# Performance work log

Measured on AMD Instinct MI355X. Metric: run time of the kernel, lower is better.

The kernel has to match this reference:

```python
import jax, jax.numpy as jnp
import numpy as np


def bilinear_align_corners(p, H, W):
    # p: [B, C, h, w] -> [B, C, H, W], matches F.interpolate(mode='bilinear', align_corners=True)
    b, c, h, w = p.shape
    ys = jnp.linspace(0.0, h - 1.0, H)
    xs = jnp.linspace(0.0, w - 1.0, W)
    y0 = jnp.floor(ys).astype(jnp.int32)
    x0 = jnp.floor(xs).astype(jnp.int32)
    y1 = jnp.minimum(y0 + 1, h - 1)
    x1 = jnp.minimum(x0 + 1, w - 1)
    wy = (ys - y0.astype(p.dtype))[:, None]          # [H,1]
    wx = (xs - x0.astype(p.dtype))                   # [W]
    rows = p[:, :, y0, :] * (1 - wy) + p[:, :, y1, :] * wy   # [B,C,H,w]
    out = rows[:, :, :, x0] * (1 - wx) + rows[:, :, :, x1] * wx  # [B,C,H,W]
    return out


def conv1x1(x, W, b):
    return jnp.einsum('bchw,oc->bohw', x, W) + b[None, :, None, None]


def scan_axis(feat, A_bar, B_bar, axis):
    # selective recurrence h_i = A_i * stop_grad(h_{i-1}) + B_i * x_i along `axis`
    f = jnp.moveaxis(feat, axis, 0)
    A = jnp.moveaxis(A_bar, axis, 0)
    B = jnp.moveaxis(B_bar, axis, 0)

    def step(prev, inp):
        a_i, b_i, x_i = inp
        h = a_i * jax.lax.stop_gradient(prev) + b_i * x_i
        return h, h

    _, hs = jax.lax.scan(step, jnp.zeros_like(f[0]), (A, B, f))
    return jnp.moveaxis(hs, 0, axis)


def setup_inputs() -> dict:
    key = jax.random.key(0)
    ks = jax.random.split(key, 12)
    Bsz, Cin, H, W = 4, 64, 256, 256
    hid = 128
    s_in = 1.0 / np.sqrt(Cin)
    s_hid = 1.0 / np.sqrt(hid)
    return {
        'x': jax.random.normal(ks[0], (Bsz, Cin, H, W), jnp.float32),
        'prior': jax.random.normal(ks[1], (Bsz, 1, 64, 64), jnp.float32),
        'W_in': jax.random.uniform(ks[2], (hid, Cin), jnp.float32, -s_in, s_in),
        'b_in': jax.random.uniform(ks[3], (hid,), jnp.float32, -s_in, s_in),
        'W_out': jax.random.uniform(ks[4], (Cin, hid), jnp.float32, -s_hid, s_hid),
        'b_out': jax.random.uniform(ks[5], (Cin,), jnp.float32, -s_hid, s_hid),
        'W_delta': jax.random.uniform(ks[6], (hid, hid), jnp.float32, -s_hid, s_hid),
        'b_delta': jax.random.uniform(ks[7], (hid,), jnp.float32, -s_hid, s_hid),
        'W_B': jax.random.uniform(ks[8], (hid, hid), jnp.float32, -s_hid, s_hid),
        'b_B': jax.random.uniform(ks[9], (hid,), jnp.float32, -s_hid, s_hid),
        'A_param': jax.random.normal(ks[10], (hid,), jnp.float32),
        'lambda_delta': jnp.float32(0.1),
        'alpha': jnp.float32(0.1),
        'gamma': jnp.float32(0.1),
    }


def reference(x, prior, W_in, b_in, W_out, b_out, W_delta, b_delta, W_B, b_B,
              A_param, lambda_delta, alpha, gamma):
    Bsz, C, H, W = x.shape
    prior_up = jnp.clip(bilinear_align_corners(prior, H, W), -1.0, 1.0)
    x_proj = conv1x1(x, W_in, b_in)
    delta = jax.nn.softplus(conv1x1(x_proj, W_delta, b_delta) + lambda_delta * prior_up)
    B_k = conv1x1(x_proj, W_B, b_B) * (1.0 + alpha * prior_up)
    A = -jnp.exp(A_param)[None, :, None, None]
    A_bar = jnp.exp(delta * A)
    B_bar = delta * B_k
    # dim=0 in torch code scans along W (axis 3); dim=1 scans along H (axis 2)
    scanned = scan_axis(x_proj, A_bar, B_bar, 3) + scan_axis(x_proj, A_bar, B_bar, 2)
    out = conv1x1(scanned, W_out, b_out)
    return (x + gamma * out, prior_up)
```

## Files before the change

### kernel.cpp

```cpp
#include <hip/hip_runtime.h>
#include <hip/hip_bf16.h>

#define OUT1 16777216
#define BIG  33554432

typedef _Float16 half8 __attribute__((ext_vector_type(8)));
typedef float    floatx4 __attribute__((ext_vector_type(4)));

struct __align__(8) h4s { _Float16 x, y, z, w; };
struct __align__(16) au16 { h4s a, u; };

__global__ __launch_bounds__(256) void k_prior(const float* __restrict__ prior, float* __restrict__ pu){
    int i = blockIdx.x*256 + threadIdx.x;
    int b = i >> 16;
    int rem = i & 65535;
    int yy = rem >> 8, xx = rem & 255;
    const float scale = 63.0f/255.0f;
    float sy = yy*scale, sx = xx*scale;
    int y0 = min((int)floorf(sy), 63), x0 = min((int)floorf(sx), 63);
    int y1 = min(y0+1, 63), x1 = min(x0+1, 63);
    float wy = sy - (float)y0, wx = sx - (float)x0;
    const float* pb = prior + (b<<12);
    float v00 = pb[(y0<<6)+x0], v01 = pb[(y0<<6)+x1];
    float v10 = pb[(y1<<6)+x0], v11 = pb[(y1<<6)+x1];
    float r0 = v00*(1.f-wy) + v10*wy;
    float r1 = v01*(1.f-wy) + v11*wy;
    float v  = r0*(1.f-wx) + r1*wx;
    pu[i] = fminf(fmaxf(v, -1.f), 1.f);
}

__global__ __launch_bounds__(256) void k_comb(const float* __restrict__ W_in, const float* __restrict__ b_in,
        const float* __restrict__ W_delta, const float* __restrict__ b_delta,
        const float* __restrict__ W_B, const float* __restrict__ b_B,
        const float* __restrict__ A_param, const float* __restrict__ W_out,
        _Float16* __restrict__ Wch, float* __restrict__ bcv, float* __restrict__ negA,
        _Float16* __restrict__ Wof, float* __restrict__ bct){
    int i = blockIdx.x*256 + threadIdx.x;
    if (i < 24576){
        int r = i >> 6, c = i & 63;
        float v;
        if (r < 128) v = W_in[i];
        else if (r < 256){
            int rr = r-128; float s = 0.f;
            for (int k=0;k<128;k++) s = fmaf(W_delta[(rr<<7)+k], W_in[(k<<6)+c], s);
            v = s;
        } else {
            int rr = r-256; float s = 0.f;
            for (int k=0;k<128;k++) s = fmaf(W_B[(rr<<7)+k], W_in[(k<<6)+c], s);
            v = s;
        }
        Wch[i] = (_Float16)v;
    } else if (i < 24960){
        int r = i - 24576; float v;
        if (r < 128) v = b_in[r];
        else if (r < 256){
            int rr=r-128; float s = b_delta[rr];
            for (int k=0;k<128;k++) s = fmaf(W_delta[(rr<<7)+k], b_in[k], s);
            v = s;
        } else {
            int rr=r-256; float s = b_B[rr];
            for (int k=0;k<128;k++) s = fmaf(W_B[(rr<<7)+k], b_in[k], s);
            v = s;
        }
        bcv[r] = v;
    } else if (i < 25088){
        negA[i-24960] = -expf(A_param[i-24960]);
    } else if (i < 33280){
        Wof[i-25088] = (_Float16)W_out[i-25088];
    } else if (i < 33792){
        int j = i - 33280;
        int c = j >> 2, comp = j & 3;
        float v;
        if (comp == 0) v = b_in[c];
        else if (comp == 1){
            float s = b_delta[c];
            for (int k=0;k<128;k++) s = fmaf(W_delta[(c<<7)+k], b_in[k], s);
            v = s;
        } else if (comp == 2){
            float s = b_B[c];
            for (int k=0;k<128;k++) s = fmaf(W_B[(c<<7)+k], b_in[k], s);
            v = s;
        } else {
            v = -expf(A_param[c]);
        }
        bct[j] = v;
    }
}

__global__ __launch_bounds__(512, 4) void k_proj_mfma(const float* __restrict__ x, const float* __restrict__ pu,
        const _Float16* __restrict__ Wch, const float* __restrict__ bct,
        const float* __restrict__ lam_p, const float* __restrict__ alp_p,
        au16* __restrict__ AU){
    __shared__ _Float16 Ws[24576];

    const int t    = threadIdx.x;
    const int lane = t & 63;
    const int wave = t >> 6;
    const int col  = lane & 15;
    const int quad = lane >> 4;

    const int bl      = blockIdx.x;
    const int b       = bl >> 7;
    const int px_base = (bl & 127) << 9;

    {
        const float4* wsrc = (const float4*)Wch;
        #pragma unroll
        for (int i = 0; i < 6; i++){
            int c = t + (i << 9);
            int row = c >> 3, part = c & 7;
            float4 v = wsrc[c];
            int byteoff = ((row << 7) + (part << 4)) ^ ((row & 7) << 4);
            *(float4*)((char*)Ws + byteoff) = v;
        }
    }

    const float lamv = lam_p[0], alpv = alp_p[0];
    const float* xcol = x + ((size_t)b<<22) + col;

    float xf0[8], xf1[8];
    {
        const float* xp = xcol + px_base + (wave<<4);
        #pragma unroll
        for (int j = 0; j < 8; j++){
            xf0[j] = xp[(size_t)(quad*8 + j) << 16];
            xf1[j] = xp[(size_t)(quad*8 + j + 32) << 16];
        }
    }

    __syncthreads();

    const int qb = quad << 4;
    const char* wsb = (const char*)Ws;

    #pragma unroll 1
    for (int ch = 0; ch < 4; ch++){
        const int pxw = px_base + (ch << 7) + (wave << 4);

        half8 aX0, aX1;
        #pragma unroll
        for (int j = 0; j < 8; j++){
            aX0[j] = (_Float16)xf0[j];
            aX1[j] = (_Float16)xf1[j];
        }

        if (ch < 3){
            const float* xn = xcol + pxw + 128;
            #pragma unroll
            for (int j = 0; j < 8; j++){
                xf0[j] = xn[(size_t)(quad*8 + j) << 16];
                xf1[j] = xn[(size_t)(quad*8 + j + 32) << 16];
            }
        }

        float4 puv4 = *(const float4*)(pu + (b<<16) + pxw + (quad<<2));
        float lpu[4], apu[4];
        #pragma unroll
        for (int r = 0; r < 4; r++){
            float pv = ((const float*)&puv4)[r];
            lpu[r] = lamv * pv;
            apu[r] = fmaf(alpv, pv, 1.f);
        }

        #pragma unroll 2
        for (int ct = 0; ct < 8; ct++){
            int rI = (ct << 4) + col;
            int xr = (rI & 7) << 4;
            half8 wI0 = *(const half8*)(wsb + ((( rI       << 7) +      qb) ^ xr));
            half8 wI1 = *(const half8*)(wsb + ((( rI       << 7) + 64 + qb) ^ xr));
            half8 wD0 = *(const half8*)(wsb + ((((rI + 128)<< 7) +      qb) ^ xr));
            half8 wD1 = *(const half8*)(wsb + ((((rI + 128)<< 7) + 64 + qb) ^ xr));
            half8 wB0 = *(const half8*)(wsb + ((((rI + 256)<< 7) +      qb) ^ xr));
            half8 wB1 = *(const half8*)(wsb + ((((rI + 256)<< 7) + 64 + qb) ^ xr));

            floatx4 aI = (floatx4){0.f,0.f,0.f,0.f};
            floatx4 aD = (floatx4){0.f,0.f,0.f,0.f};
            floatx4 aB = (floatx4){0.f,0.f,0.f,0.f};
            aI = __builtin_amdgcn_mfma_f32_16x16x32_f16(aX0, wI0, aI, 0, 0, 0);
            aD = __builtin_amdgcn_mfma_f32_16x16x32_f16(aX0, wD0, aD, 0, 0, 0);
            aB = __builtin_amdgcn_mfma_f32_16x16x32_f16(aX0, wB0, aB, 0, 0, 0);
            aI = __builtin_amdgcn_mfma_f32_16x16x32_f16(aX1, wI1, aI, 0, 0, 0);
            aD = __builtin_amdgcn_mfma_f32_16x16x32_f16(aX1, wD1, aD, 0, 0, 0);
            aB = __builtin_amdgcn_mfma_f32_16x16x32_f16(aX1, wB1, aB, 0, 0, 0);

            int c = (ct<<4) + col;
            float4 bv = *(const float4*)(bct + (c<<2));
            au16 ov;
            #pragma unroll
            for (int r = 0; r < 4; r++){
                float sI = aI[r] + bv.x;
                float sD = aD[r] + bv.y;
                float sB = aB[r] + bv.z;
                float dpre  = sD + lpu[r];
                float delta = fmaxf(dpre, 0.f) + __logf(1.f + __expf(-fabsf(dpre)));
                float ab    = __expf(bv.w * delta);
                float uu    = delta * sB * apu[r] * sI;
                (&ov.a.x)[r] = (_Float16)ab;
                (&ov.u.x)[r] = (_Float16)uu;
            }
            size_t u = (((size_t)((b<<7) + c)) << 14) + (pxw >> 2) + quad;
            AU[u] = ov;
        }
    }
}

__global__ __launch_bounds__(512) void k_scan_wh(const au16* __restrict__ AU, _Float16* __restrict__ Sh){
    __shared__ float As[8][256], Us[8][256], Wsc[8][256];
    __shared__ _Float16 Shs[8][256];

    const int t    = threadIdx.x;
    const int lane = t & 63;
    const int wave = t >> 6;
    const size_t plane = (size_t)blockIdx.x;

    float Hcol = 0.f;

    const size_t ub = (plane << 14) + (wave << 6) + lane;

    au16 cA = AU[ub];
    au16 cB = AU[ub + 512];

    auto proc = [&](au16 cur, int gg){
        float ax=(float)cur.a.x, ay=(float)cur.a.y, az=(float)cur.a.z, aw=(float)cur.a.w;
        float ux=(float)cur.u.x, uy=(float)cur.u.y, uz=(float)cur.u.z, uw=(float)cur.u.w;

        float A = ax, U = ux;
        U = fmaf(ay, U, uy); A *= ay;
        U = fmaf(az, U, uz); A *= az;
        U = fmaf(aw, U, uw); A *= aw;
        #pragma unroll
        for (int off=1; off<64; off<<=1){
            float Apv = __shfl_up(A, off, 64);
            float Upv = __shfl_up(U, off, 64);
            if (lane >= off){ U = fmaf(A, Upv, U); A *= Apv; }
        }
        float h = __shfl_up(U, 1, 64);
        if (lane == 0) h = 0.f;
        float4 o;
        h = fmaf(ax, h, ux); o.x = h;
        h = fmaf(ay, h, uy); o.y = h;
        h = fmaf(az, h, uz); o.z = h;
        h = fmaf(aw, h, uw); o.w = h;

        int c0 = lane << 2;
        *(float4*)&As [wave][c0] = (float4){ax,ay,az,aw};
        *(float4*)&Us [wave][c0] = (float4){ux,uy,uz,uw};
        *(float4*)&Wsc[wave][c0] = o;

        asm volatile("s_waitcnt lgkmcnt(0)" ::: "memory");
        __builtin_amdgcn_sched_barrier(0);
        __builtin_amdgcn_s_barrier();
        __builtin_amdgcn_sched_barrier(0);

        if (t < 256){
            #pragma unroll
            for (int v = 0; v < 8; v++){
                Hcol = fmaf(As[v][t], Hcol, Us[v][t]);
                Shs[v][t] = (_Float16)(Hcol + Wsc[v][t]);
            }
        }

        asm volatile("s_waitcnt lgkmcnt(0)" ::: "memory");
        __builtin_amdgcn_sched_barrier(0);
        __builtin_amdgcn_s_barrier();
        __builtin_amdgcn_sched_barrier(0);

        h4s sv = *(h4s*)&Shs[wave][lane << 2];
        *(h4s*)(Sh + (plane << 16) + ((size_t)((gg << 3) + wave) << 8) + (lane << 2)) = sv;
    };

    #pragma unroll 1
    for (int g = 0; g < 32; g += 2){
        proc(cA, g);
        if (g + 2 < 32) cA = AU[ub + (size_t)(g + 2) * 512];
        proc(cB, g + 1);
        if (g + 3 < 32) cB = AU[ub + (size_t)(g + 3) * 512];
    }
}

__global__ __launch_bounds__(256, 4) void k_out_mfma(const float* __restrict__ x, const _Float16* __restrict__ Sh,
        const _Float16* __restrict__ Wof, const float* __restrict__ bout, const float* __restrict__ gam_p,
        float* __restrict__ out){
    const int t    = threadIdx.x;
    const int lane = t & 63;
    const int wave = t >> 6;
    const int col  = lane & 15;
    const int quad = lane >> 4;
    const int b    = blockIdx.x >> 8;
    const int p0   = (blockIdx.x & 255) << 8;
    const int wn0  = wave << 6;

    const _Float16* shb = Sh + ((size_t)b<<23) + p0 + wn0;

    floatx4 acc[4][4];
    #pragma unroll
    for (int mt = 0; mt < 4; mt++)
        #pragma unroll
        for (int nt = 0; nt < 4; nt++)
            acc[mt][nt] = (floatx4){0.f,0.f,0.f,0.f};

    #pragma unroll
    for (int kc = 0; kc < 4; kc++){
        half8 af[4];
        #pragma unroll
        for (int mt = 0; mt < 4; mt++)
            #pragma unroll
            for (int j = 0; j < 8; j++)
                af[mt][j] = shb[((size_t)(kc*32 + quad*8 + j)<<16) + mt*16 + col];
        half8 bf[4];
        #pragma unroll
        for (int nt = 0; nt < 4; nt++)
            bf[nt] = *(const half8*)(Wof + (nt*16 + col)*128 + kc*32 + quad*8);
        #pragma unroll
        for (int mt = 0; mt < 4; mt++)
            #pragma unroll
            for (int nt = 0; nt < 4; nt++)
                acc[mt][nt] = __builtin_amdgcn_mfma_f32_16x16x32_f16(af[mt], bf[nt], acc[mt][nt], 0, 0, 0);
    }

    const float gv = gam_p[0];
    #pragma unroll
    for (int nt = 0; nt < 4; nt++){
        int o = nt*16 + col;
        float bo = bout[o];
        #pragma unroll
        for (int mt = 0; mt < 4; mt++){
            size_t idx = (((size_t)(b*64 + o))<<16) + p0 + wn0 + mt*16 + (quad<<2);
            float4 xv = *(const float4*)(x + idx);
            float4 ov;
            ov.x = fmaf(gv, acc[mt][nt][0] + bo, xv.x);
            ov.y = fmaf(gv, acc[mt][nt][1] + bo, xv.y);
            ov.z = fmaf(gv, acc[mt][nt][2] + bo, xv.z);
            ov.w = fmaf(gv, acc[mt][nt][3] + bo, xv.w);
            *(float4*)(out + idx) = ov;
        }
    }
}

extern "C" void kernel_launch(void* const* d_in, const int* in_sizes, int n_in,
                              void* d_out, int out_size, void* d_ws, size_t ws_size,
                              hipStream_t stream){
    const float* x       = (const float*)d_in[0];
    const float* prior   = (const float*)d_in[1];
    const float* W_in    = (const float*)d_in[2];
    const float* b_in    = (const float*)d_in[3];
    const float* W_out   = (const float*)d_in[4];
    const float* b_out   = (const float*)d_in[5];
    const float* W_delta = (const float*)d_in[6];
    const float* b_delta = (const float*)d_in[7];
    const float* W_B     = (const float*)d_in[8];
    const float* b_B     = (const float*)d_in[9];
    const float* A_param = (const float*)d_in[10];
    const float* lam     = (const float*)d_in[11];
    const float* alp     = (const float*)d_in[12];
    const float* gam     = (const float*)d_in[13];

    float* out = (float*)d_out;
    float* pu  = out + OUT1;

    float* ws        = (float*)d_ws;
    _Float16* Wch    = (_Float16*)ws;
    float* bcv       = ws + 12288;
    float* negA      = ws + 12672;
    _Float16* Wof    = (_Float16*)(ws + 12800);
    float* bct       = ws + 16896;
    au16* AU         = (au16*)(ws + 32768);
    _Float16* Sh     = (_Float16*)(AU + BIG/4);

    hipLaunchKernelGGL(k_prior,  dim3(1024),  dim3(256), 0, stream, prior, pu);
    hipLaunchKernelGGL(k_comb,   dim3(132),   dim3(256), 0, stream, W_in, b_in, W_delta, b_delta,
                       W_B, b_B, A_param, W_out, Wch, bcv, negA, Wof, bct);
    hipLaunchKernelGGL(k_proj_mfma, dim3(512), dim3(512), 0, stream,
                       x, pu, Wch, bct, lam, alp, AU);
    hipLaunchKernelGGL(k_scan_wh, dim3(512), dim3(512), 0, stream, AU, Sh);
    hipLaunchKernelGGL(k_out_mfma, dim3(1024), dim3(256), 0, stream, x, Sh, Wof, b_out, gam, out);
}
```

Before: 272.5 us.

## Fuse prior upsampling into projection and transpose scan output layout

Removes the standalone prior-upsampling kernel and computes the clipped bilinear prior inline in the projection kernel, also writing it to the output there. The scan's intermediate buffer is reordered from batch-channel-row-column to batch-row-channel-column. This lets each output-projection block read one contiguous region instead of channel planes spread far apart. It trades redundant per-lane prior computation and stores for one fewer launch and better read locality.

```diff
diff --git a/kernel.cpp b/kernel.cpp
--- a/kernel.cpp
+++ b/kernel.cpp
@@ -9,25 +9,6 @@
 
 struct __align__(8) h4s { _Float16 x, y, z, w; };
 struct __align__(16) au16 { h4s a, u; };
-
-__global__ __launch_bounds__(256) void k_prior(const float* __restrict__ prior, float* __restrict__ pu){
-    int i = blockIdx.x*256 + threadIdx.x;
-    int b = i >> 16;
-    int rem = i & 65535;
-    int yy = rem >> 8, xx = rem & 255;
-    const float scale = 63.0f/255.0f;
-    float sy = yy*scale, sx = xx*scale;
-    int y0 = min((int)floorf(sy), 63), x0 = min((int)floorf(sx), 63);
-    int y1 = min(y0+1, 63), x1 = min(x0+1, 63);
-    float wy = sy - (float)y0, wx = sx - (float)x0;
-    const float* pb = prior + (b<<12);
-    float v00 = pb[(y0<<6)+x0], v01 = pb[(y0<<6)+x1];
-    float v10 = pb[(y1<<6)+x0], v11 = pb[(y1<<6)+x1];
-    float r0 = v00*(1.f-wy) + v10*wy;
-    float r1 = v01*(1.f-wy) + v11*wy;
-    float v  = r0*(1.f-wx) + r1*wx;
-    pu[i] = fminf(fmaxf(v, -1.f), 1.f);
-}
 
 __global__ __launch_bounds__(256) void k_comb(const float* __restrict__ W_in, const float* __restrict__ b_in,
         const float* __restrict__ W_delta, const float* __restrict__ b_delta,
@@ -87,10 +68,10 @@
     }
 }
 
-__global__ __launch_bounds__(512, 4) void k_proj_mfma(const float* __restrict__ x, const float* __restrict__ pu,
+__global__ __launch_bounds__(512, 4) void k_proj_mfma(const float* __restrict__ x, const float* __restrict__ prior,
         const _Float16* __restrict__ Wch, const float* __restrict__ bct,
         const float* __restrict__ lam_p, const float* __restrict__ alp_p,
-        au16* __restrict__ AU){
+        float* __restrict__ pu, au16* __restrict__ AU){
     __shared__ _Float16 Ws[24576];
 
     const int t    = threadIdx.x;
@@ -153,14 +134,31 @@
             }
         }
 
-        float4 puv4 = *(const float4*)(pu + (b<<16) + pxw + (quad<<2));
+        const float scale = 63.0f/255.0f;
+        int yy = pxw >> 8;
+        float sy = yy*scale;
+        int y0 = min((int)floorf(sy), 63);
+        int y1 = min(y0+1, 63);
+        float wy = sy - (float)y0;
+        const float* pb0 = prior + (b<<12) + (y0<<6);
+        const float* pb1 = prior + (b<<12) + (y1<<6);
+        int xx0 = (pxw & 255) + (quad<<2);
         float lpu[4], apu[4];
+        float4 puo;
         #pragma unroll
         for (int r = 0; r < 4; r++){
-            float pv = ((const float*)&puv4)[r];
+            float sx = (float)(xx0 + r)*scale;
+            int x0 = min((int)floorf(sx), 63);
+            int x1 = min(x0+1, 63);
+            float wx = sx - (float)x0;
+            float r0 = pb0[x0]*(1.f-wy) + pb1[x0]*wy;
+            float r1 = pb0[x1]*(1.f-wy) + pb1[x1]*wy;
+            float pv = fminf(fmaxf(r0*(1.f-wx) + r1*wx, -1.f), 1.f);
+            ((float*)&puo)[r] = pv;
             lpu[r] = lamv * pv;
             apu[r] = fmaf(alpv, pv, 1.f);
         }
+        *(float4*)(pu + (b<<16) + pxw + (quad<<2)) = puo;
 
         #pragma unroll 2
         for (int ct = 0; ct < 8; ct++){
@@ -212,6 +210,7 @@
     const int lane = t & 63;
     const int wave = t >> 6;
     const size_t plane = (size_t)blockIdx.x;
+    const size_t bI = plane >> 7, cI = plane & 127;
 
     float Hcol = 0.f;
 
@@ -266,7 +265,8 @@
         __builtin_amdgcn_sched_barrier(0);
 
         h4s sv = *(h4s*)&Shs[wave][lane << 2];
-        *(h4s*)(Sh + (plane << 16) + ((size_t)((gg << 3) + wave) << 8) + (lane << 2)) = sv;
+        size_t hh = (size_t)((gg << 3) + wave);
+        *(h4s*)(Sh + (bI<<23) + (hh<<15) + (cI<<8) + (lane<<2)) = sv;
     };
 
     #pragma unroll 1
@@ -287,10 +287,11 @@
     const int col  = lane & 15;
     const int quad = lane >> 4;
     const int b    = blockIdx.x >> 8;
-    const int p0   = (blockIdx.x & 255) << 8;
+    const int hh   = blockIdx.x & 255;
+    const int p0   = hh << 8;
     const int wn0  = wave << 6;
 
-    const _Float16* shb = Sh + ((size_t)b<<23) + p0 + wn0;
+    const _Float16* shb = Sh + ((size_t)b<<23) + ((size_t)hh<<15);
 
     floatx4 acc[4][4];
     #pragma unroll
@@ -306,7 +307,7 @@
         for (int mt = 0; mt < 4; mt++)
             #pragma unroll
             for (int j = 0; j < 8; j++)
-                af[mt][j] = shb[((size_t)(kc*32 + quad*8 + j)<<16) + mt*16 + col];
+                af[mt][j] = shb[((kc*32 + quad*8 + j)<<8) + wn0 + mt*16 + col];
         half8 bf[4];
         #pragma unroll
         for (int nt = 0; nt < 4; nt++)
@@ -367,11 +368,10 @@
     au16* AU         = (au16*)(ws + 32768);
     _Float16* Sh     = (_Float16*)(AU + BIG/4);
 
-    hipLaunchKernelGGL(k_prior,  dim3(1024),  dim3(256), 0, stream, prior, pu);
     hipLaunchKernelGGL(k_comb,   dim3(132),   dim3(256), 0, stream, W_in, b_in, W_delta, b_delta,
                        W_B, b_B, A_param, W_out, Wch, bcv, negA, Wof, bct);
     hipLaunchKernelGGL(k_proj_mfma, dim3(512), dim3(512), 0, stream,
-                       x, pu, Wch, bct, lam, alp, AU);
+                       x, prior, Wch, bct, lam, alp, pu, AU);
     hipLaunchKernelGGL(k_scan_wh, dim3(512), dim3(512), 0, stream, AU, Sh);
     hipLaunchKernelGGL(k_out_mfma, dim3(1024), dim3(256), 0, stream, x, Sh, Wof, b_out, gam, out);
 }
```

Result: no change. 273.6 us (+0.4%).
